# Performance work log

Measured on AMD Instinct MI355X. Metric: run time of the kernel, lower is better.

The kernel has to match this reference:

```python
import jax, jax.numpy as jnp
import numpy as np
from jax import lax

B, N, C, H = 8, 1024, 384, 6
D = C // H
SCALE = D ** -0.5
EPS = 1e-5


def setup_inputs() -> dict:
    key = jax.random.key(0)
    ks = jax.random.split(key, 10)
    s = 0.02
    return {
        "x": jax.random.normal(ks[0], (B, N, C), jnp.float32),
        "w_qkv": jax.random.normal(ks[1], (3 * C, C), jnp.float32) * s,
        "w_proj": jax.random.normal(ks[2], (C, C), jnp.float32) * s,
        "b_proj": jax.random.normal(ks[3], (C,), jnp.float32) * s,
        "w_kq": jax.random.normal(ks[4], (H, 1, 3, 3), jnp.float32) * 0.1,   # depthwise (groups=H)
        "b_kq": jax.random.normal(ks[5], (H,), jnp.float32) * 0.1,
        "w_head": jax.random.normal(ks[6], (H, H, 1, 1), jnp.float32) * 0.1,  # 1x1 head-mixing conv
        "b_head": jax.random.normal(ks[7], (H,), jnp.float32) * 0.1,
        "gn_w": jnp.ones((H,), jnp.float32),
        "gn_b": jnp.zeros((H,), jnp.float32),
    }


def reference(x, w_qkv, w_proj, b_proj, w_kq, b_kq, w_head, b_head, gn_w, gn_b):
    # qkv projection (torch Linear: y = x @ W.T)
    qkv = (x @ w_qkv.T).reshape(B, N, 3, H, D).transpose(2, 0, 3, 1, 4)  # [3,B,H,N,D]
    q, k, v = qkv[0], qkv[1], qkv[2]

    # attention logits [B,H,N,N]
    logits = jnp.einsum("bhnd,bhmd->bhnm", q, k) * SCALE

    # depthwise (groups=H) 3x3 conv over the NxN logit map
    logits = lax.conv_general_dilated(
        logits, w_kq, window_strides=(1, 1), padding=((1, 1), (1, 1)),
        dimension_numbers=("NCHW", "OIHW", "NCHW"), feature_group_count=H,
    ) + b_kq[None, :, None, None]

    attn = jax.nn.softmax(logits, axis=-1)

    # 1x1 conv mixing heads
    attn = jnp.einsum("oh,bhnm->bonm", w_head[:, :, 0, 0], attn) + b_head[None, :, None, None]

    # GroupNorm(num_groups=H, channels=H): per (b, head) stats over NxN
    mean = attn.mean(axis=(2, 3), keepdims=True)
    var = ((attn - mean) ** 2).mean(axis=(2, 3), keepdims=True)
    attn = (attn - mean) * lax.rsqrt(var + EPS)
    attn = attn * gn_w[None, :, None, None] + gn_b[None, :, None, None]

    out = jnp.einsum("bhnm,bhmd->bhnd", attn, v)
    out = out.transpose(0, 2, 1, 3).reshape(B, N, C)
    return out @ w_proj.T + b_proj
```

## Files before the change

kernel.cpp:

```cpp
#include <hip/hip_runtime.h>

typedef unsigned short u16;
typedef __attribute__((ext_vector_type(8))) short short8;
typedef __attribute__((ext_vector_type(4))) float f32x4;

#define MFMA(a, b, c) __builtin_amdgcn_mfma_f32_16x16x32_bf16((a), (b), (c), 0, 0, 0)

__device__ inline float bf2f(u16 u) {
  union { unsigned int i; float f; } w; w.i = ((unsigned int)u) << 16; return w.f;
}
__device__ inline u16 f2bf(float x) {
  union { float f; unsigned int i; } u; u.f = x;
  unsigned int r = u.i + 0x7fffu + ((u.i >> 16) & 1u);
  return (u16)(r >> 16);
}
__device__ inline unsigned int pk2(float a, float b) {
  return (unsigned int)f2bf(a) | ((unsigned int)f2bf(b) << 16);
}
__device__ inline void unpack8(uint4 v, float* f) {
  union { unsigned int i; float g; } c;
  c.i = v.x << 16;          f[0] = c.g;
  c.i = v.x & 0xffff0000u;  f[1] = c.g;
  c.i = v.y << 16;          f[2] = c.g;
  c.i = v.y & 0xffff0000u;  f[3] = c.g;
  c.i = v.z << 16;          f[4] = c.g;
  c.i = v.z & 0xffff0000u;  f[5] = c.g;
  c.i = v.w << 16;          f[6] = c.g;
  c.i = v.w & 0xffff0000u;  f[7] = c.g;
}

static const size_t SZ_QKV = (size_t)48 * 1024 * 64 * 2;
static const size_t SZ_MAP = (size_t)48 * 1024 * 1024 * 2;
static const size_t OFF_Q  = 0;
static const size_t OFF_K  = OFF_Q + SZ_QKV;
static const size_t OFF_VT = OFF_K + SZ_QKV;
static const size_t OFF_S  = OFF_VT + SZ_QKV;
static const size_t OFF_UG = OFF_S;
static const size_t OFF_QM = OFF_S + SZ_MAP;
static const size_t OFF_OT = OFF_QM + SZ_MAP;
static const size_t OFF_ST = OFF_OT + SZ_QKV;
static const size_t OFF_CS = OFF_ST + 896;

__global__ __launch_bounds__(256, 3) void k_qkv(const float* __restrict__ x,
                                                const float* __restrict__ w,
                                                u16* __restrict__ qb,
                                                u16* __restrict__ kb,
                                                u16* __restrict__ vT,
                                                float* __restrict__ colsum) {
  __shared__ u16 SH[16384];
  u16* As = SH;
  u16* Bs = SH + 8192;
  const int t = threadIdx.x;
  const int m0 = blockIdx.x * 128;
  const int n0 = blockIdx.y * 128;
  const int wave = t >> 6, lane = t & 63;
  const int wm = (wave & 1) * 64, wn = (wave >> 1) * 64;
  const int fr = lane & 15;
  const int fk = (lane >> 4) * 8;
  f32x4 acc[4][4] = {};
  for (int k0 = 0; k0 < 384; k0 += 64) {
#pragma unroll
    for (int i = 0; i < 4; ++i) {
      int e = (i * 256 + t) * 8;
      int row = e >> 6, col = e & 63;
      const float* xp = &x[(size_t)(m0 + row) * 384 + k0 + col];
      const float* wp = &w[(size_t)(n0 + row) * 384 + k0 + col];
      float4 a0 = *(const float4*)xp, a1 = *(const float4*)(xp + 4);
      uint4 av; av.x = pk2(a0.x, a0.y); av.y = pk2(a0.z, a0.w);
      av.z = pk2(a1.x, a1.y); av.w = pk2(a1.z, a1.w);
      *(uint4*)&As[e] = av;
      float4 b0 = *(const float4*)wp, b1 = *(const float4*)(wp + 4);
      uint4 bv; bv.x = pk2(b0.x, b0.y); bv.y = pk2(b0.z, b0.w);
      bv.z = pk2(b1.x, b1.y); bv.w = pk2(b1.z, b1.w);
      *(uint4*)&Bs[e] = bv;
    }
    __syncthreads();
#pragma unroll
    for (int ks = 0; ks < 2; ++ks) {
      const int ko = ks * 32 + fk;
      short8 a[4], b[4];
#pragma unroll
      for (int mi = 0; mi < 4; ++mi) a[mi] = *(const short8*)&As[(wm + mi * 16 + fr) * 64 + ko];
#pragma unroll
      for (int ni = 0; ni < 4; ++ni) b[ni] = *(const short8*)&Bs[(wn + ni * 16 + fr) * 64 + ko];
#pragma unroll
      for (int mi = 0; mi < 4; ++mi)
#pragma unroll
        for (int ni = 0; ni < 4; ++ni) acc[mi][ni] = MFMA(a[mi], b[ni], acc[mi][ni]);
    }
    __syncthreads();
  }
  u16* st = &SH[wave * 4096];
  const int gcb = n0 + wn;
  const int s = gcb / 384;
  const int remb = gcb - s * 384;
  const int h = remb >> 6;
#pragma unroll
  for (int mi = 0; mi < 4; ++mi)
#pragma unroll
    for (int ni = 0; ni < 4; ++ni)
#pragma unroll
      for (int r = 0; r < 4; ++r) {
        int rl = mi * 16 + (lane >> 4) * 4 + r;
        int cl = ni * 16 + fr;
        u16 val = f2bf(acc[mi][ni][r]);
        if (s == 2) st[cl * 64 + rl] = val;
        else        st[rl * 64 + cl] = val;
      }
  const int gm0 = m0 + wm;
  const int b_ = gm0 >> 10;
  const size_t base = (size_t)(b_ * 6 + h) << 16;
  const int nloc = gm0 & 1023;
  const int r8 = lane >> 3, c8 = (lane & 7) * 8;
#pragma unroll
  for (int i = 0; i < 8; ++i) {
    int lrow = i * 8 + r8;
    uint4 v = *(const uint4*)&st[lrow * 64 + c8];
    if (s == 0)      *(uint4*)&qb[base + (size_t)(nloc + lrow) * 64 + c8] = v;
    else if (s == 1) *(uint4*)&kb[base + (size_t)(nloc + lrow) * 64 + c8] = v;
    else             *(uint4*)&vT[base + (size_t)lrow * 1024 + nloc + c8] = v;
  }
  if (s == 2) {
#pragma unroll
    for (int ni = 0; ni < 4; ++ni) {
      float p = 0.f;
#pragma unroll
      for (int mi = 0; mi < 4; ++mi)
#pragma unroll
        for (int r = 0; r < 4; ++r) p += bf2f(f2bf(acc[mi][ni][r]));
      p += __shfl_xor(p, 16, 64);
      p += __shfl_xor(p, 32, 64);
      if ((lane >> 4) == 0)
        atomicAdd(&colsum[(b_ * 6 + h) * 64 + ni * 16 + fr], p);
    }
  }
}

__global__ __launch_bounds__(256, 3) void k_qk(const u16* __restrict__ qb,
                                               const u16* __restrict__ kb,
                                               u16* __restrict__ S) {
  __shared__ u16 SH[16384];
  u16* As = SH;
  u16* Bs = SH + 8192;
  const int t = threadIdx.x;
  const int m0 = blockIdx.x * 128, n0 = blockIdx.y * 128;
  const int bh = blockIdx.z;
  const u16* A = qb + ((size_t)bh << 16);
  const u16* Bp = kb + ((size_t)bh << 16);
  const int wave = t >> 6, lane = t & 63;
  const int wm = (wave & 1) * 64, wn = (wave >> 1) * 64;
  const int fr = lane & 15;
  const int fk = (lane >> 4) * 8;
  f32x4 acc[4][4] = {};
#pragma unroll
  for (int i = 0; i < 4; ++i) {
    int e = (i * 256 + t) * 8;
    *(uint4*)&As[e] = *(const uint4*)&A[(size_t)m0 * 64 + e];
    *(uint4*)&Bs[e] = *(const uint4*)&Bp[(size_t)n0 * 64 + e];
  }
  __syncthreads();
#pragma unroll
  for (int ks = 0; ks < 2; ++ks) {
    const int ko = ks * 32 + fk;
    short8 a[4], b[4];
#pragma unroll
    for (int mi = 0; mi < 4; ++mi) a[mi] = *(const short8*)&As[(wm + mi * 16 + fr) * 64 + ko];
#pragma unroll
    for (int ni = 0; ni < 4; ++ni) b[ni] = *(const short8*)&Bs[(wn + ni * 16 + fr) * 64 + ko];
#pragma unroll
    for (int mi = 0; mi < 4; ++mi)
#pragma unroll
      for (int ni = 0; ni < 4; ++ni) acc[mi][ni] = MFMA(a[mi], b[ni], acc[mi][ni]);
  }
  __syncthreads();
  u16* st = &SH[wave * 4096];
#pragma unroll
  for (int mi = 0; mi < 4; ++mi)
#pragma unroll
    for (int ni = 0; ni < 4; ++ni)
#pragma unroll
      for (int r = 0; r < 4; ++r)
        st[(mi * 16 + (lane >> 4) * 4 + r) * 64 + ni * 16 + fr] = f2bf(acc[mi][ni][r] * 0.125f);
  const size_t sb = (size_t)bh << 20;
  const int grow0 = m0 + wm, gcol0 = n0 + wn;
  const int r8 = lane >> 3, c8 = (lane & 7) * 8;
#pragma unroll
  for (int i = 0; i < 8; ++i) {
    int lrow = i * 8 + r8;
    uint4 v = *(const uint4*)&st[lrow * 64 + c8];
    *(uint4*)&S[sb + (size_t)(grow0 + lrow) * 1024 + gcol0 + c8] = v;
  }
}

__global__ __launch_bounds__(256) void k_conv_softmax(const u16* __restrict__ S,
                                                      const float* __restrict__ w_kq,
                                                      u16* __restrict__ Qb) {
  __shared__ u16 Sr[10 * 1040];
  __shared__ float red[4];
  const int t = threadIdx.x;
  const int bh = blockIdx.y;
  const int h = bh % 6;
  const int r0 = blockIdx.x * 8;
  const u16* Sp = S + ((size_t)bh << 20);
  float wv[9];
#pragma unroll
  for (int i = 0; i < 9; ++i) wv[i] = w_kq[h * 9 + i];
  if (t < 10) { Sr[t * 1040 + 7] = 0; Sr[t * 1040 + 1032] = 0; }
#pragma unroll
  for (int c = 0; c < 5; ++c) {
    int e = (c * 256 + t) * 8;
    int i = e >> 10, col = e & 1023;
    int g = r0 - 1 + i;
    uint4 val = make_uint4(0u, 0u, 0u, 0u);
    if (g >= 0 && g < 1024) val = *(const uint4*)&Sp[(size_t)g * 1024 + col];
    *(uint4*)&Sr[i * 1040 + 8 + col] = val;
  }
  __syncthreads();
  const int half = t >> 7;
  const int lane = t & 63;
  const int m0 = (t & 127) * 8;
  for (int pass = 0; pass < 4; ++pass) {
    int rr = pass * 2 + half;
    float o8[8];
#pragma unroll
    for (int j = 0; j < 8; ++j) o8[j] = 0.f;
#pragma unroll
    for (int i = 0; i < 3; ++i) {
      const u16* rowp = &Sr[(rr + i) * 1040 + 8];
      float left = bf2f(rowp[m0 - 1]);
      float md[8];
      unpack8(*(const uint4*)&rowp[m0], md);
      float right = bf2f(rowp[m0 + 8]);
      float w0 = wv[i * 3 + 0], w1 = wv[i * 3 + 1], w2 = wv[i * 3 + 2];
      o8[0] += w0 * left + w1 * md[0] + w2 * md[1];
#pragma unroll
      for (int j = 1; j < 7; ++j) o8[j] += w0 * md[j - 1] + w1 * md[j] + w2 * md[j + 1];
      o8[7] += w0 * md[6] + w1 * md[7] + w2 * right;
    }
    float mx = o8[0];
#pragma unroll
    for (int j = 1; j < 8; ++j) mx = fmaxf(mx, o8[j]);
    for (int off = 32; off; off >>= 1) mx = fmaxf(mx, __shfl_xor(mx, off, 64));
    if (lane == 0) red[t >> 6] = mx;
    __syncthreads();
    float rmax = fmaxf(red[half * 2], red[half * 2 + 1]);
    __syncthreads();
    float e8[8], s = 0.f;
#pragma unroll
    for (int j = 0; j < 8; ++j) { e8[j] = __expf(o8[j] - rmax); s += e8[j]; }
    for (int off = 32; off; off >>= 1) s += __shfl_xor(s, off, 64);
    if (lane == 0) red[t >> 6] = s;
    __syncthreads();
    float rsum = red[half * 2] + red[half * 2 + 1];
    __syncthreads();
    float scale = 1024.f / rsum;
    unsigned int pk[4];
#pragma unroll
    for (int jj = 0; jj < 4; ++jj)
      pk[jj] = pk2(e8[2 * jj] * scale - 1.f, e8[2 * jj + 1] * scale - 1.f);
    int n = r0 + rr;
    *(uint4*)&Qb[((size_t)bh << 20) + (size_t)n * 1024 + m0] = make_uint4(pk[0], pk[1], pk[2], pk[3]);
  }
}

__global__ __launch_bounds__(256) void k_pvmix(const u16* __restrict__ Qm,
                                               const u16* __restrict__ vT,
                                               const float* __restrict__ wh,
                                               float* __restrict__ Ug,
                                               float* __restrict__ stats) {
  __shared__ u16 SH[2 * 64 * 72];
  u16* Am = SH;
  u16* Vm = SH + 64 * 72;
  const int t = threadIdx.x;
  const int bid = blockIdx.x;
  const int b_ = bid & 7;
  const int sidx = bid >> 3;
  const int n0 = (sidx / 6) * 64;
  const int o = sidx % 6;
  const int bo = b_ * 6 + o;
  const int wave = t >> 6, lane = t & 63;
  const int fr = lane & 15, quad = lane >> 4;
  const int srow = t >> 3, smg8 = (t & 7) * 8;
  float wo[6];
#pragma unroll
  for (int hh = 0; hh < 6; ++hh) wo[hh] = wh[o * 6 + hh];
  const size_t qbase = ((size_t)(b_ * 6)) << 20;
  const u16* vp = vT + ((size_t)bo << 16);
  uint4 qpre[2][6];
  uint4 vpre[2];
  {
    const int m = smg8;
#pragma unroll
    for (int i = 0; i < 2; ++i)
#pragma unroll
      for (int hh = 0; hh < 6; ++hh)
        qpre[i][hh] = *(const uint4*)&Qm[qbase + (((size_t)hh) << 20) +
                                         (size_t)(n0 + i * 32 + srow) * 1024 + m];
    vpre[0] = *(const uint4*)&vp[(size_t)srow * 1024 + m];
    vpre[1] = *(const uint4*)&vp[(size_t)(32 + srow) * 1024 + m];
  }
  f32x4 acc[4] = {};
  float s1 = 0.f, s2 = 0.f;
  for (int mc = 0; mc < 16; ++mc) {
    __syncthreads();
#pragma unroll
    for (int i = 0; i < 2; ++i) {
      float mix[8] = {0.f, 0.f, 0.f, 0.f, 0.f, 0.f, 0.f, 0.f};
#pragma unroll
      for (int hh = 0; hh < 6; ++hh) {
        float qf[8];
        unpack8(qpre[i][hh], qf);
        float w = wo[hh];
#pragma unroll
        for (int j = 0; j < 8; ++j) mix[j] += w * qf[j];
      }
#pragma unroll
      for (int j = 0; j < 8; ++j) { s1 += mix[j]; s2 += mix[j] * mix[j]; }
      uint4 pk4;
      pk4.x = pk2(mix[0], mix[1]); pk4.y = pk2(mix[2], mix[3]);
      pk4.z = pk2(mix[4], mix[5]); pk4.w = pk2(mix[6], mix[7]);
      *(uint4*)&Am[(i * 32 + srow) * 72 + smg8] = pk4;
    }
    *(uint4*)&Vm[srow * 72 + smg8] = vpre[0];
    *(uint4*)&Vm[(32 + srow) * 72 + smg8] = vpre[1];
    if (mc < 15) {
      const int m = (mc + 1) * 64 + smg8;
#pragma unroll
      for (int i = 0; i < 2; ++i)
#pragma unroll
        for (int hh = 0; hh < 6; ++hh)
          qpre[i][hh] = *(const uint4*)&Qm[qbase + (((size_t)hh) << 20) +
                                           (size_t)(n0 + i * 32 + srow) * 1024 + m];
      vpre[0] = *(const uint4*)&vp[(size_t)srow * 1024 + m];
      vpre[1] = *(const uint4*)&vp[(size_t)(32 + srow) * 1024 + m];
    }
    __syncthreads();
#pragma unroll
    for (int ks = 0; ks < 2; ++ks) {
      short8 a = *(const short8*)&Am[(wave * 16 + fr) * 72 + ks * 32 + quad * 8];
#pragma unroll
      for (int ni = 0; ni < 4; ++ni) {
        short8 b = *(const short8*)&Vm[(ni * 16 + fr) * 72 + ks * 32 + quad * 8];
        acc[ni] = MFMA(a, b, acc[ni]);
      }
    }
  }
  __syncthreads();
  float* FS = (float*)SH;
#pragma unroll
  for (int ni = 0; ni < 4; ++ni)
#pragma unroll
    for (int r = 0; r < 4; ++r)
      FS[(wave * 16 + quad * 4 + r) * 64 + ni * 16 + fr] = acc[ni][r];
  __syncthreads();
  float* Up = Ug + ((size_t)(bo * 1024 + n0)) * 64;
#pragma unroll
  for (int j = 0; j < 4; ++j) {
    int oo = j * 1024 + t * 4;
    *(float4*)&Up[oo] = *(const float4*)&FS[oo];
  }
  for (int off = 32; off; off >>= 1) {
    s1 += __shfl_xor(s1, off, 64);
    s2 += __shfl_xor(s2, off, 64);
  }
  if (lane == 0) {
    atomicAdd(&stats[bo * 2 + 0], s1);
    atomicAdd(&stats[bo * 2 + 1], s2);
  }
}

__global__ __launch_bounds__(256) void k_apply(const float* __restrict__ Ug,
                                               const float* __restrict__ stats,
                                               const float* __restrict__ colsum,
                                               const float* __restrict__ gn_w,
                                               const float* __restrict__ gn_b,
                                               u16* __restrict__ otmp) {
  int i = blockIdx.x * 256 + threadIdx.x;
  int e = i * 4;
  int d4 = e & 63;
  int n = (e >> 6) & 1023;
  int bo = e >> 16;
  int b = bo / 6, o = bo - b * 6;
  float s1 = stats[bo * 2], s2 = stats[bo * 2 + 1];
  const float inv = 1.f / 1048576.f;
  float mu = s1 * inv;
  float var = s2 * inv - mu * mu;
  float alpha = gn_w[o] * rsqrtf(var + 1e-5f * 1048576.f);
  float beta = gn_b[o] - alpha * mu;
  float4 cs = *(const float4*)&colsum[bo * 64 + d4];
  float4 u = *(const float4*)&Ug[e];
  uint2 w;
  w.x = pk2(alpha * u.x + beta * cs.x, alpha * u.y + beta * cs.y);
  w.y = pk2(alpha * u.z + beta * cs.z, alpha * u.w + beta * cs.w);
  *(uint2*)&otmp[((size_t)(b * 1024 + n)) * 384 + o * 64 + d4] = w;
}

__global__ __launch_bounds__(256, 3) void k_proj(const u16* __restrict__ A,
                                                 const float* __restrict__ w,
                                                 const float* __restrict__ bias,
                                                 float* __restrict__ out) {
  __shared__ u16 SH[16384];
  u16* As = SH;
  u16* Bs = SH + 8192;
  const int t = threadIdx.x;
  const int m0 = blockIdx.x * 128;
  const int n0 = blockIdx.y * 128;
  const int wave = t >> 6, lane = t & 63;
  const int wm = (wave & 1) * 64, wn = (wave >> 1) * 64;
  const int fr = lane & 15;
  const int fk = (lane >> 4) * 8;
  f32x4 acc[4][4] = {};
  for (int k0 = 0; k0 < 384; k0 += 64) {
#pragma unroll
    for (int i = 0; i < 4; ++i) {
      int e = (i * 256 + t) * 8;
      int row = e >> 6, col = e & 63;
      *(uint4*)&As[e] = *(const uint4*)&A[(size_t)(m0 + row) * 384 + k0 + col];
      const float* wp = &w[(size_t)(n0 + row) * 384 + k0 + col];
      float4 b0 = *(const float4*)wp, b1 = *(const float4*)(wp + 4);
      uint4 bv; bv.x = pk2(b0.x, b0.y); bv.y = pk2(b0.z, b0.w);
      bv.z = pk2(b1.x, b1.y); bv.w = pk2(b1.z, b1.w);
      *(uint4*)&Bs[e] = bv;
    }
    __syncthreads();
#pragma unroll
    for (int ks = 0; ks < 2; ++ks) {
      const int ko = ks * 32 + fk;
      short8 a[4], b[4];
#pragma unroll
      for (int mi = 0; mi < 4; ++mi) a[mi] = *(const short8*)&As[(wm + mi * 16 + fr) * 64 + ko];
#pragma unroll
      for (int ni = 0; ni < 4; ++ni) b[ni] = *(const short8*)&Bs[(wn + ni * 16 + fr) * 64 + ko];
#pragma unroll
      for (int mi = 0; mi < 4; ++mi)
#pragma unroll
        for (int ni = 0; ni < 4; ++ni) acc[mi][ni] = MFMA(a[mi], b[ni], acc[mi][ni]);
    }
    __syncthreads();
  }
  float* FS = (float*)SH;
  float* fst = &FS[wave * 2048];
  float bv[4];
#pragma unroll
  for (int ni = 0; ni < 4; ++ni) bv[ni] = bias[n0 + wn + ni * 16 + fr];
#pragma unroll
  for (int half = 0; half < 2; ++half) {
#pragma unroll
    for (int mi2 = 0; mi2 < 2; ++mi2) {
      int mi = half * 2 + mi2;
#pragma unroll
      for (int ni = 0; ni < 4; ++ni)
#pragma unroll
        for (int r = 0; r < 4; ++r)
          fst[(mi2 * 16 + (lane >> 4) * 4 + r) * 64 + ni * 16 + fr] = acc[mi][ni][r] + bv[ni];
    }
#pragma unroll
    for (int g = 0; g < 4; ++g)
#pragma unroll
      for (int i2 = 0; i2 < 2; ++i2) {
        int lrow = g * 8 + (lane >> 3);
        int colf = i2 * 32 + (lane & 7) * 4;
        float4 v = *(const float4*)&fst[lrow * 64 + colf];
        *(float4*)&out[(size_t)(m0 + wm + half * 32 + lrow) * 384 + n0 + wn + colf] = v;
      }
  }
}

extern "C" void kernel_launch(void* const* d_in, const int* in_sizes, int n_in,
                              void* d_out, int out_size, void* d_ws, size_t ws_size,
                              hipStream_t stream) {
  (void)in_sizes; (void)n_in; (void)out_size; (void)ws_size;
  const float* x      = (const float*)d_in[0];
  const float* w_qkv  = (const float*)d_in[1];
  const float* w_proj = (const float*)d_in[2];
  const float* b_proj = (const float*)d_in[3];
  const float* w_kq   = (const float*)d_in[4];
  const float* w_head = (const float*)d_in[6];
  const float* gn_w   = (const float*)d_in[8];
  const float* gn_b   = (const float*)d_in[9];

  char* ws = (char*)d_ws;
  u16*   qb      = (u16*)(ws + OFF_Q);
  u16*   kb      = (u16*)(ws + OFF_K);
  u16*   vT      = (u16*)(ws + OFF_VT);
  u16*   Sb      = (u16*)(ws + OFF_S);
  float* Ug      = (float*)(ws + OFF_UG);
  u16*   Qm      = (u16*)(ws + OFF_QM);
  u16*   otmp    = (u16*)(ws + OFF_OT);
  float* stats   = (float*)(ws + OFF_ST);
  float* colsum  = (float*)(ws + OFF_CS);

  hipMemsetAsync(stats, 0, 896 + 12288, stream);
  k_qkv<<<dim3(64, 9), 256, 0, stream>>>(x, w_qkv, qb, kb, vT, colsum);
  k_qk<<<dim3(8, 8, 48), 256, 0, stream>>>(qb, kb, Sb);
  k_conv_softmax<<<dim3(128, 48), 256, 0, stream>>>(Sb, w_kq, Qm);
  k_pvmix<<<dim3(768), 256, 0, stream>>>(Qm, vT, w_head, Ug, stats);
  k_apply<<<dim3(3072), 256, 0, stream>>>(Ug, stats, colsum, gn_w, gn_b, otmp);
  k_proj<<<dim3(64, 3), 256, 0, stream>>>(otmp, w_proj, b_proj, (float*)d_out);
}
```

Before: 275.6 us.

## Fuse QK^T logits computation into conv+softmax kernel, dropping S map round-trip

Merges the QK^T GEMM and the depthwise-conv/softmax kernels. Each block recomputes a band of 16 logit rows (14 output rows plus a one-row halo on each side) straight into shared memory, streaming K in 64-row chunks through registers. This removes the write and reread of the full bf16 logit map (about 100 MB) and one launch. In exchange it recomputes the halo rows, runs small 16-row MFMA tiles with many barriers, and uses 7 passes per block instead of 4.

```diff
diff --git a/kernel.cpp b/kernel.cpp
--- a/kernel.cpp
+++ b/kernel.cpp
@@ -34,9 +34,8 @@
 static const size_t OFF_Q  = 0;
 static const size_t OFF_K  = OFF_Q + SZ_QKV;
 static const size_t OFF_VT = OFF_K + SZ_QKV;
-static const size_t OFF_S  = OFF_VT + SZ_QKV;
-static const size_t OFF_UG = OFF_S;
-static const size_t OFF_QM = OFF_S + SZ_MAP;
+static const size_t OFF_UG = OFF_VT + SZ_QKV;
+static const size_t OFF_QM = OFF_UG + SZ_MAP;
 static const size_t OFF_OT = OFF_QM + SZ_MAP;
 static const size_t OFF_ST = OFF_OT + SZ_QKV;
 static const size_t OFF_CS = OFF_ST + 896;
@@ -136,90 +135,67 @@
   }
 }
 
-__global__ __launch_bounds__(256, 3) void k_qk(const u16* __restrict__ qb,
-                                               const u16* __restrict__ kb,
-                                               u16* __restrict__ S) {
-  __shared__ u16 SH[16384];
-  u16* As = SH;
-  u16* Bs = SH + 8192;
-  const int t = threadIdx.x;
-  const int m0 = blockIdx.x * 128, n0 = blockIdx.y * 128;
-  const int bh = blockIdx.z;
-  const u16* A = qb + ((size_t)bh << 16);
-  const u16* Bp = kb + ((size_t)bh << 16);
-  const int wave = t >> 6, lane = t & 63;
-  const int wm = (wave & 1) * 64, wn = (wave >> 1) * 64;
-  const int fr = lane & 15;
-  const int fk = (lane >> 4) * 8;
-  f32x4 acc[4][4] = {};
-#pragma unroll
-  for (int i = 0; i < 4; ++i) {
-    int e = (i * 256 + t) * 8;
-    *(uint4*)&As[e] = *(const uint4*)&A[(size_t)m0 * 64 + e];
-    *(uint4*)&Bs[e] = *(const uint4*)&Bp[(size_t)n0 * 64 + e];
-  }
-  __syncthreads();
-#pragma unroll
-  for (int ks = 0; ks < 2; ++ks) {
-    const int ko = ks * 32 + fk;
-    short8 a[4], b[4];
-#pragma unroll
-    for (int mi = 0; mi < 4; ++mi) a[mi] = *(const short8*)&As[(wm + mi * 16 + fr) * 64 + ko];
-#pragma unroll
-    for (int ni = 0; ni < 4; ++ni) b[ni] = *(const short8*)&Bs[(wn + ni * 16 + fr) * 64 + ko];
-#pragma unroll
-    for (int mi = 0; mi < 4; ++mi)
-#pragma unroll
-      for (int ni = 0; ni < 4; ++ni) acc[mi][ni] = MFMA(a[mi], b[ni], acc[mi][ni]);
-  }
-  __syncthreads();
-  u16* st = &SH[wave * 4096];
-#pragma unroll
-  for (int mi = 0; mi < 4; ++mi)
-#pragma unroll
-    for (int ni = 0; ni < 4; ++ni)
-#pragma unroll
-      for (int r = 0; r < 4; ++r)
-        st[(mi * 16 + (lane >> 4) * 4 + r) * 64 + ni * 16 + fr] = f2bf(acc[mi][ni][r] * 0.125f);
-  const size_t sb = (size_t)bh << 20;
-  const int grow0 = m0 + wm, gcol0 = n0 + wn;
-  const int r8 = lane >> 3, c8 = (lane & 7) * 8;
-#pragma unroll
-  for (int i = 0; i < 8; ++i) {
-    int lrow = i * 8 + r8;
-    uint4 v = *(const uint4*)&st[lrow * 64 + c8];
-    *(uint4*)&S[sb + (size_t)(grow0 + lrow) * 1024 + gcol0 + c8] = v;
-  }
-}
-
-__global__ __launch_bounds__(256) void k_conv_softmax(const u16* __restrict__ S,
-                                                      const float* __restrict__ w_kq,
-                                                      u16* __restrict__ Qb) {
-  __shared__ u16 Sr[10 * 1040];
+__global__ __launch_bounds__(256) void k_qkconv(const u16* __restrict__ qb,
+                                                const u16* __restrict__ kb,
+                                                const float* __restrict__ w_kq,
+                                                u16* __restrict__ Qb) {
+  __shared__ u16 Sr[16 * 1040];
+  __shared__ u16 Qs[16 * 68];
+  __shared__ u16 Ks[64 * 68];
   __shared__ float red[4];
   const int t = threadIdx.x;
-  const int bh = blockIdx.y;
-  const int h = bh % 6;
-  const int r0 = blockIdx.x * 8;
-  const u16* Sp = S + ((size_t)bh << 20);
+  const int bid = blockIdx.x;
+  const int b_ = bid & 7;
+  const int rest = bid >> 3;
+  const int h = rest % 6;
+  const int band = rest / 6;
+  const int bh = b_ * 6 + h;
+  const int n0 = band * 14;
+  const int wave = t >> 6, lane = t & 63;
+  const int fr = lane & 15, quad = lane >> 4;
+
+  if (t < 128) {
+    int i = t >> 3, c8 = (t & 7) * 8;
+    int g = n0 - 1 + i;
+    uint4 val = make_uint4(0u, 0u, 0u, 0u);
+    if (g >= 0 && g < 1024)
+      val = *(const uint4*)&qb[((size_t)bh << 16) + (size_t)g * 64 + c8];
+    *(uint4*)&Qs[i * 68 + c8] = val;
+  }
+  if (t < 16) { Sr[t * 1040 + 7] = 0; Sr[t * 1040 + 1032] = 0; }
+  const u16* kp = kb + ((size_t)bh << 16);
+  uint4 kreg0 = *(const uint4*)&kp[(size_t)(t >> 3) * 64 + (t & 7) * 8];
+  uint4 kreg1 = *(const uint4*)&kp[(size_t)(32 + (t >> 3)) * 64 + (t & 7) * 8];
+
+  for (int c = 0; c < 16; ++c) {
+    __syncthreads();
+    *(uint4*)&Ks[(t >> 3) * 68 + (t & 7) * 8] = kreg0;
+    *(uint4*)&Ks[((t >> 3) + 32) * 68 + (t & 7) * 8] = kreg1;
+    if (c < 15) {
+      const size_t ro = (size_t)(c + 1) * 64 * 64;
+      kreg0 = *(const uint4*)&kp[ro + (size_t)(t >> 3) * 64 + (t & 7) * 8];
+      kreg1 = *(const uint4*)&kp[ro + (size_t)(32 + (t >> 3)) * 64 + (t & 7) * 8];
+    }
+    __syncthreads();
+    f32x4 acc = {};
+#pragma unroll
+    for (int ks = 0; ks < 2; ++ks) {
+      short8 a = *(const short8*)&Qs[fr * 68 + ks * 32 + quad * 8];
+      short8 bfr = *(const short8*)&Ks[(wave * 16 + fr) * 68 + ks * 32 + quad * 8];
+      acc = MFMA(a, bfr, acc);
+    }
+#pragma unroll
+    for (int r = 0; r < 4; ++r)
+      Sr[(quad * 4 + r) * 1040 + 8 + c * 64 + wave * 16 + fr] = f2bf(acc[r] * 0.125f);
+  }
+  __syncthreads();
+
   float wv[9];
 #pragma unroll
   for (int i = 0; i < 9; ++i) wv[i] = w_kq[h * 9 + i];
-  if (t < 10) { Sr[t * 1040 + 7] = 0; Sr[t * 1040 + 1032] = 0; }
-#pragma unroll
-  for (int c = 0; c < 5; ++c) {
-    int e = (c * 256 + t) * 8;
-    int i = e >> 10, col = e & 1023;
-    int g = r0 - 1 + i;
-    uint4 val = make_uint4(0u, 0u, 0u, 0u);
-    if (g >= 0 && g < 1024) val = *(const uint4*)&Sp[(size_t)g * 1024 + col];
-    *(uint4*)&Sr[i * 1040 + 8 + col] = val;
-  }
-  __syncthreads();
   const int half = t >> 7;
-  const int lane = t & 63;
   const int m0 = (t & 127) * 8;
-  for (int pass = 0; pass < 4; ++pass) {
+  for (int pass = 0; pass < 7; ++pass) {
     int rr = pass * 2 + half;
     float o8[8];
 #pragma unroll
@@ -254,12 +230,14 @@
     float rsum = red[half * 2] + red[half * 2 + 1];
     __syncthreads();
     float scale = 1024.f / rsum;
-    unsigned int pk[4];
-#pragma unroll
-    for (int jj = 0; jj < 4; ++jj)
-      pk[jj] = pk2(e8[2 * jj] * scale - 1.f, e8[2 * jj + 1] * scale - 1.f);
-    int n = r0 + rr;
-    *(uint4*)&Qb[((size_t)bh << 20) + (size_t)n * 1024 + m0] = make_uint4(pk[0], pk[1], pk[2], pk[3]);
+    int n = n0 + rr;
+    if (n < 1024) {
+      unsigned int pk[4];
+#pragma unroll
+      for (int jj = 0; jj < 4; ++jj)
+        pk[jj] = pk2(e8[2 * jj] * scale - 1.f, e8[2 * jj + 1] * scale - 1.f);
+      *(uint4*)&Qb[((size_t)bh << 20) + (size_t)n * 1024 + m0] = make_uint4(pk[0], pk[1], pk[2], pk[3]);
+    }
   }
 }
 
@@ -483,7 +461,6 @@
   u16*   qb      = (u16*)(ws + OFF_Q);
   u16*   kb      = (u16*)(ws + OFF_K);
   u16*   vT      = (u16*)(ws + OFF_VT);
-  u16*   Sb      = (u16*)(ws + OFF_S);
   float* Ug      = (float*)(ws + OFF_UG);
   u16*   Qm      = (u16*)(ws + OFF_QM);
   u16*   otmp    = (u16*)(ws + OFF_OT);
@@ -492,8 +469,7 @@
 
   hipMemsetAsync(stats, 0, 896 + 12288, stream);
   k_qkv<<<dim3(64, 9), 256, 0, stream>>>(x, w_qkv, qb, kb, vT, colsum);
-  k_qk<<<dim3(8, 8, 48), 256, 0, stream>>>(qb, kb, Sb);
-  k_conv_softmax<<<dim3(128, 48), 256, 0, stream>>>(Sb, w_kq, Qm);
+  k_qkconv<<<dim3(3552), 256, 0, stream>>>(qb, kb, w_kq, Qm);
   k_pvmix<<<dim3(768), 256, 0, stream>>>(Qm, vT, w_head, Ug, stats);
   k_apply<<<dim3(3072), 256, 0, stream>>>(Ug, stats, colsum, gn_w, gn_b, otmp);
   k_proj<<<dim3(64, 3), 256, 0, stream>>>(otmp, w_proj, b_proj, (float*)d_out);
```

Result: no change. 275.2 us (-0.1%).
